# Optimization experiments

Measured on AMD Instinct MI355X. Metric: run time of the kernel, lower is better.

The kernel has to match this reference:

```python
import jax, jax.numpy as jnp
import numpy as np

B, NQ, NK, D, H, DFF = 4, 1024, 1024, 1024, 16, 4096
DH = D // H
SCALE = 1.0 / np.sqrt(D).astype(np.float32)  # torch code scales by sqrt(dim_V), not head_dim
LN_EPS = 1e-5


def setup_inputs() -> dict:
    key = jax.random.key(0)
    ks = jax.random.split(key, 20)
    s = lambda fan_in: 1.0 / np.sqrt(fan_in).astype(np.float32)
    inp = {
        "Q": jax.random.normal(ks[0], (B, NQ, D), jnp.float32),
        "K": jax.random.normal(ks[1], (B, NK, D), jnp.float32),
        # attention projections (torch Linear stored here as [in, out])
        "Wq": jax.random.uniform(ks[2], (D, D), jnp.float32, -s(D), s(D)),
        "bq": jnp.zeros((D,), jnp.float32),
        "Wk": jax.random.uniform(ks[3], (D, D), jnp.float32, -s(D), s(D)),
        "bk": jnp.zeros((D,), jnp.float32),
        "Wv": jax.random.uniform(ks[4], (D, D), jnp.float32, -s(D), s(D)),
        "bv": jnp.zeros((D,), jnp.float32),
        "Wo": jax.random.uniform(ks[5], (D, D), jnp.float32, -s(D), s(D)),
        "bo": jnp.zeros((D,), jnp.float32),
        # FFN
        "W1": jax.random.uniform(ks[6], (D, DFF), jnp.float32, -s(D), s(D)),
        "b1": jnp.zeros((DFF,), jnp.float32),
        "W2": jax.random.uniform(ks[7], (DFF, D), jnp.float32, -s(DFF), s(DFF)),
        "b2": jnp.zeros((D,), jnp.float32),
        # LayerNorms
        "g0": jnp.ones((D,), jnp.float32),
        "be0": jnp.zeros((D,), jnp.float32),
        "g1": jnp.ones((D,), jnp.float32),
        "be1": jnp.zeros((D,), jnp.float32),
    }
    return inp


def _layernorm(x, g, b):
    mu = x.mean(-1, keepdims=True)
    var = ((x - mu) ** 2).mean(-1, keepdims=True)
    return (x - mu) * jax.lax.rsqrt(var + LN_EPS) * g + b


def reference(Q, K, Wq, bq, Wk, bk, Wv, bv, Wo, bo, W1, b1, W2, b2, g0, be0, g1, be1):
    # multi-head attention (MHA path, mask=None)
    q = (Q @ Wq + bq).reshape(B, NQ, H, DH)
    k = (K @ Wk + bk).reshape(B, NK, H, DH)
    v = (K @ Wv + bv).reshape(B, NK, H, DH)
    E = jnp.einsum("bqhd,bkhd->bhqk", q, k) * SCALE  # [B,H,NQ,NK]
    A = jax.nn.softmax(E, axis=-1)
    O = jnp.einsum("bhqk,bkhd->bqhd", A, v).reshape(B, NQ, D)
    O = O @ Wo + bo
    # residual + LN0
    X = _layernorm(Q + O, g0, be0)
    # FFN + residual + LN1
    Y = jnp.maximum(X @ W1 + b1, 0.0) @ W2 + b2
    return _layernorm(X + Y, g1, be1)
```

## Files before the change

kernel.cpp:

```cpp
#include <hip/hip_runtime.h>
#include <math.h>

#define B_   4
#define NQ_  1024
#define NK_  1024
#define D_   1024
#define H_   16
#define DH_  64
#define DFF_ 4096
#define SCALE_ (1.0f/32.0f)
#define LN_EPS_ 1e-5f

typedef __attribute__((ext_vector_type(8))) short bf16x8_t;
typedef __attribute__((ext_vector_type(4))) float f32x4_t;

__device__ __forceinline__ ushort f2bf_rne(float x) {
    unsigned u = __float_as_uint(x);
    unsigned r = (u + 0x7FFFu + ((u >> 16) & 1u)) >> 16;
    return (ushort)r;
}
__device__ __forceinline__ float bf2f(ushort h) {
    return __uint_as_float(((unsigned)h) << 16);
}

__device__ __forceinline__ void gl_lds16(const ushort* g, ushort* l) {
    __builtin_amdgcn_global_load_lds(
        (const __attribute__((address_space(1))) unsigned int*)g,
        (__attribute__((address_space(3))) unsigned int*)l, 16, 0, 0);
}

__global__ __launch_bounds__(256) void split_rows(const float* __restrict__ src,
        ushort* __restrict__ hi, ushort* __restrict__ lo, int n4)
{
    int i = blockIdx.x * 256 + threadIdx.x;
    if (i >= n4) return;
    float4 v = ((const float4*)src)[i];
    ushort4 h, l;
    h.x = f2bf_rne(v.x); l.x = f2bf_rne(v.x - bf2f(h.x));
    h.y = f2bf_rne(v.y); l.y = f2bf_rne(v.y - bf2f(h.y));
    h.z = f2bf_rne(v.z); l.z = f2bf_rne(v.z - bf2f(h.z));
    h.w = f2bf_rne(v.w); l.w = f2bf_rne(v.w - bf2f(h.w));
    ((ushort4*)hi)[i] = h;
    ((ushort4*)lo)[i] = l;
}

__global__ __launch_bounds__(256) void split_tr(const float* __restrict__ Wsrc,
        ushort* __restrict__ th, ushort* __restrict__ tl, int K, int N)
{
    __shared__ float tile[32][33];
    const int nb = blockIdx.x * 32, kb = blockIdx.y * 32;
    const int t = threadIdx.x;
    {
        int r = t >> 3, c4 = (t & 7) * 4;
        float4 v = *(const float4*)&Wsrc[(size_t)(kb + r) * N + nb + c4];
        tile[r][c4 + 0] = v.x; tile[r][c4 + 1] = v.y;
        tile[r][c4 + 2] = v.z; tile[r][c4 + 3] = v.w;
    }
    __syncthreads();
    {
        int n = t >> 3, k4 = (t & 7) * 4;
        float a0 = tile[k4 + 0][n], a1 = tile[k4 + 1][n];
        float a2 = tile[k4 + 2][n], a3 = tile[k4 + 3][n];
        ushort4 h, l;
        h.x = f2bf_rne(a0); l.x = f2bf_rne(a0 - bf2f(h.x));
        h.y = f2bf_rne(a1); l.y = f2bf_rne(a1 - bf2f(h.y));
        h.z = f2bf_rne(a2); l.z = f2bf_rne(a2 - bf2f(h.z));
        h.w = f2bf_rne(a3); l.w = f2bf_rne(a3 - bf2f(h.w));
        size_t o = (size_t)(nb + n) * K + kb + k4;
        *(ushort4*)&th[o] = h;
        *(ushort4*)&tl[o] = l;
    }
}

__device__ __forceinline__ void swz_block(int& brow, int& bcol, int tile) {
    const int nx  = gridDim.x;
    const int lin = blockIdx.y * nx + blockIdx.x;
    const int cpx = (nx * gridDim.y) >> 3;
    const int swz = (lin & 7) * cpx + (lin >> 3);
    brow = (swz / nx) * tile;
    bcol = (swz % nx) * tile;
}

template<bool RELU, int OMODE>
__device__ __forceinline__ void gemm_body(
        const ushort* __restrict__ Ah, const ushort* __restrict__ Al,
        const ushort* __restrict__ Bh, const ushort* __restrict__ Bl,
        const float* __restrict__ bias,
        float* __restrict__ C, ushort* __restrict__ Ch, ushort* __restrict__ Cl,
        int M, int N, int Kd, int Klen, int brow, int bcol)
{
    __shared__ __align__(16) ushort S[2][4][128 * 32];

    const int t    = threadIdx.x;
    const int lane = t & 63;
    const int w    = t >> 6;
    const int wr   = (w >> 1) * 64;
    const int wc   = (w & 1) * 64;
    const int fr   = lane & 15;
    const int g    = lane >> 4;
    const int sS   = ((g ^ ((fr >> 1) & 3)) << 3);
    const int cl   = lane & 15;
    const int rq   = (lane >> 4) * 4;

    float bpre[4];
    #pragma unroll
    for (int j = 0; j < 4; ++j)
        bpre[j] = bias ? bias[bcol + wc + j * 16 + cl] : 0.f;

    f32x4_t acc[4][4];
    #pragma unroll
    for (int i = 0; i < 4; ++i)
        #pragma unroll
        for (int j = 0; j < 4; ++j)
            acc[i][j] = (f32x4_t){0.f, 0.f, 0.f, 0.f};

    const int lrow  = lane >> 2;
    const int lslot = ((lane & 3) ^ ((lane >> 3) & 3)) << 3;
    const int c0    = w * 2;

    auto issue2 = [&](const ushort* gpp, int rb, int pl, int buf, int k0) {
        #pragma unroll
        for (int ii = 0; ii < 2; ++ii) {
            int c = c0 + ii;
            gl_lds16(gpp + (size_t)(rb + c * 16 + lrow) * Kd + k0 + lslot,
                     &S[buf][pl][c * 512]);
        }
    };

    bf16x8_t ahf[4], bhf[4], blf[4], alf[4];

    issue2(Ah, brow, 0, 0, 0);
    issue2(Bh, bcol, 2, 0, 0);
    issue2(Bl, bcol, 3, 0, 0);
    issue2(Al, brow, 1, 0, 0);
    asm volatile("s_waitcnt vmcnt(4)" ::: "memory");
    __builtin_amdgcn_s_barrier();

    const int NT = Klen >> 5;
    for (int tt = 0; tt < NT; ++tt) {
        const int cur = tt & 1, nxt = cur ^ 1;
        const int kn  = (tt + 1) << 5;
        const bool more = (tt + 1 < NT);

        #pragma unroll
        for (int i = 0; i < 4; ++i)
            ahf[i] = *(const bf16x8_t*)&S[cur][0][(wr + i * 16 + fr) * 32 + sS];
        #pragma unroll
        for (int j = 0; j < 4; ++j)
            bhf[j] = *(const bf16x8_t*)&S[cur][2][(wc + j * 16 + fr) * 32 + sS];
        if (more) {
            issue2(Ah, brow, 0, nxt, kn);
            issue2(Bh, bcol, 2, nxt, kn);
            asm volatile("s_waitcnt vmcnt(6)" ::: "memory");
        } else {
            asm volatile("s_waitcnt vmcnt(2)" ::: "memory");
        }
        __builtin_amdgcn_s_barrier();
        asm volatile("s_waitcnt lgkmcnt(0)" ::: "memory");
        __builtin_amdgcn_sched_barrier(0);
        __builtin_amdgcn_s_setprio(1);
        #pragma unroll
        for (int i = 0; i < 4; ++i)
            #pragma unroll
            for (int j = 0; j < 4; ++j)
                acc[i][j] = __builtin_amdgcn_mfma_f32_16x16x32_bf16(ahf[i], bhf[j], acc[i][j], 0, 0, 0);
        __builtin_amdgcn_s_setprio(0);
        __builtin_amdgcn_s_barrier();

        #pragma unroll
        for (int j = 0; j < 4; ++j)
            blf[j] = *(const bf16x8_t*)&S[cur][3][(wc + j * 16 + fr) * 32 + sS];
        if (more) {
            issue2(Bl, bcol, 3, nxt, kn);
            asm volatile("s_waitcnt vmcnt(6)" ::: "memory");
        } else {
            asm volatile("s_waitcnt vmcnt(0)" ::: "memory");
        }
        __builtin_amdgcn_s_barrier();
        asm volatile("s_waitcnt lgkmcnt(0)" ::: "memory");
        __builtin_amdgcn_sched_barrier(0);
        __builtin_amdgcn_s_setprio(1);
        #pragma unroll
        for (int i = 0; i < 4; ++i)
            #pragma unroll
            for (int j = 0; j < 4; ++j)
                acc[i][j] = __builtin_amdgcn_mfma_f32_16x16x32_bf16(ahf[i], blf[j], acc[i][j], 0, 0, 0);
        __builtin_amdgcn_s_setprio(0);
        __builtin_amdgcn_s_barrier();

        #pragma unroll
        for (int i = 0; i < 4; ++i)
            alf[i] = *(const bf16x8_t*)&S[cur][1][(wr + i * 16 + fr) * 32 + sS];
        if (more) {
            issue2(Al, brow, 1, nxt, kn);
            asm volatile("s_waitcnt vmcnt(4)" ::: "memory");
        }
        __builtin_amdgcn_s_barrier();
        asm volatile("s_waitcnt lgkmcnt(0)" ::: "memory");
        __builtin_amdgcn_sched_barrier(0);
        __builtin_amdgcn_s_setprio(1);
        #pragma unroll
        for (int i = 0; i < 4; ++i)
            #pragma unroll
            for (int j = 0; j < 4; ++j)
                acc[i][j] = __builtin_amdgcn_mfma_f32_16x16x32_bf16(alf[i], bhf[j], acc[i][j], 0, 0, 0);
        __builtin_amdgcn_s_setprio(0);
        __builtin_amdgcn_s_barrier();
    }

    if (OMODE == 0) {
        #pragma unroll
        for (int j = 0; j < 4; ++j) {
            int col = bcol + wc + j * 16 + cl;
            #pragma unroll
            for (int i = 0; i < 4; ++i)
                #pragma unroll
                for (int r = 0; r < 4; ++r) {
                    int row = brow + wr + i * 16 + rq + r;
                    float v = acc[i][j][r] + bpre[j];
                    if (RELU) v = fmaxf(v, 0.f);
                    C[(size_t)row * N + col] = v;
                }
        }
    } else {
        float* E = (float*)&S[0][0][0] + w * 4096;
        #pragma unroll
        for (int j = 0; j < 4; ++j) {
            #pragma unroll
            for (int i = 0; i < 4; ++i)
                #pragma unroll
                for (int r = 0; r < 4; ++r) {
                    float v = acc[i][j][r] + bpre[j];
                    if (RELU) v = fmaxf(v, 0.f);
                    E[(i * 16 + rq + r) * 64 + j * 16 + cl] = v;
                }
        }
        __syncthreads();
        const int rr8 = lane >> 3;
        const int c8  = (lane & 7) * 8;
        #pragma unroll
        for (int p = 0; p < 8; ++p) {
            int rl = p * 8 + rr8;
            float4 va = *(float4*)&E[rl * 64 + c8];
            float4 vb = *(float4*)&E[rl * 64 + c8 + 4];
            float v[8] = {va.x, va.y, va.z, va.w, vb.x, vb.y, vb.z, vb.w};
            bf16x8_t hv, lv;
            #pragma unroll
            for (int q = 0; q < 8; ++q) {
                ushort hh = f2bf_rne(v[q]);
                hv[q] = (short)hh;
                lv[q] = (short)f2bf_rne(v[q] - bf2f(hh));
            }
            size_t o = (size_t)(brow + wr + rl) * N + (bcol + wc + c8);
            *(bf16x8_t*)&Ch[o] = hv;
            if (OMODE == 1) *(bf16x8_t*)&Cl[o] = lv;
        }
    }
}

template<bool RELU, int OMODE>
__global__ __launch_bounds__(256) void gemm_mfma(
        const ushort* __restrict__ Ah, const ushort* __restrict__ Al,
        const ushort* __restrict__ Bh, const ushort* __restrict__ Bl,
        const float* __restrict__ bias,
        float* __restrict__ C, ushort* __restrict__ Ch, ushort* __restrict__ Cl,
        int M, int N, int Kd)
{
    int brow, bcol;
    swz_block(brow, bcol, 128);
    gemm_body<RELU, OMODE>(Ah, Al, Bh, Bl, bias, C, Ch, Cl, M, N, Kd, Kd, brow, bcol);
}

__global__ __launch_bounds__(256) void gemm_splitk2(
        const ushort* __restrict__ Ah, const ushort* __restrict__ Al,
        const ushort* __restrict__ Bh, const ushort* __restrict__ Bl,
        const float* __restrict__ bias,
        float* __restrict__ C0, float* __restrict__ C1,
        int M, int N, int Kd)
{
    int brow, bcol;
    swz_block(brow, bcol, 128);
    const int z = blockIdx.z;
    const int Kh2 = Kd >> 1;
    const int ko  = z * Kh2;
    gemm_body<false, 0>(Ah + ko, Al + ko, Bh + ko, Bl + ko,
                        z == 0 ? bias : nullptr,
                        z == 0 ? C0 : C1, nullptr, nullptr,
                        M, N, Kd, Kh2, brow, bcol);
}

struct QkvArgs {
    const ushort* Ah[3]; const ushort* Al[3];
    const ushort* Bh[3]; const ushort* Bl[3];
    const float*  bias[3];
    ushort*       Co[3];
};

__global__ __launch_bounds__(256) void gemm_qkv(QkvArgs qa, int M, int N, int Kd)
{
    int brow, bcol;
    swz_block(brow, bcol, 128);
    const int z = blockIdx.z;
    gemm_body<false, 2>(qa.Ah[z], qa.Al[z], qa.Bh[z], qa.Bl[z], qa.bias[z],
                        nullptr, qa.Co[z], nullptr, M, N, Kd, Kd, brow, bcol);
}

__global__ __launch_bounds__(512) void gemm_ffn1_256(
        const ushort* __restrict__ Ah, const ushort* __restrict__ Al,
        const ushort* __restrict__ Bh, const ushort* __restrict__ Bl,
        const float* __restrict__ bias,
        ushort* __restrict__ Ch, ushort* __restrict__ Cl,
        int M, int N, int Kd)
{
    __shared__ __align__(16) ushort S[2][4][256 * 32];

    const int t    = threadIdx.x;
    const int lane = t & 63;
    const int w    = t >> 6;
    const int wr   = (w >> 2) * 128;
    const int wc   = (w & 3) * 64;
    const int fr   = lane & 15;
    const int g    = lane >> 4;
    const int sS   = ((g ^ ((fr >> 1) & 3)) << 3);
    const int cl   = lane & 15;
    const int rq   = (lane >> 4) * 4;

    int brow, bcol;
    swz_block(brow, bcol, 256);

    float bpre[4];
    #pragma unroll
    for (int j = 0; j < 4; ++j) bpre[j] = bias[bcol + wc + j * 16 + cl];

    f32x4_t acc[8][4];
    #pragma unroll
    for (int i = 0; i < 8; ++i)
        #pragma unroll
        for (int j = 0; j < 4; ++j)
            acc[i][j] = (f32x4_t){0.f, 0.f, 0.f, 0.f};

    const int lrow  = lane >> 2;
    const int lslot = ((lane & 3) ^ ((lane >> 3) & 3)) << 3;
    const int c0    = w * 2;

    auto issue2 = [&](const ushort* gpp, int rb, int pl, int buf, int k0) {
        #pragma unroll
        for (int ii = 0; ii < 2; ++ii) {
            int c = c0 + ii;
            gl_lds16(gpp + (size_t)(rb + c * 16 + lrow) * Kd + k0 + lslot,
                     &S[buf][pl][c * 512]);
        }
    };

    bf16x8_t ahf[8], bhf[4], blf[4], alf[8];

    issue2(Ah, brow, 0, 0, 0);
    issue2(Bh, bcol, 2, 0, 0);
    issue2(Bl, bcol, 3, 0, 0);
    issue2(Al, brow, 1, 0, 0);
    asm volatile("s_waitcnt vmcnt(4)" ::: "memory");
    __builtin_amdgcn_s_barrier();

    const int NT = Kd >> 5;
    for (int tt = 0; tt < NT; ++tt) {
        const int cur = tt & 1, nxt = cur ^ 1;
        const int kn  = (tt + 1) << 5;
        const bool more = (tt + 1 < NT);

        #pragma unroll
        for (int i = 0; i < 8; ++i)
            ahf[i] = *(const bf16x8_t*)&S[cur][0][(wr + i * 16 + fr) * 32 + sS];
        #pragma unroll
        for (int j = 0; j < 4; ++j)
            bhf[j] = *(const bf16x8_t*)&S[cur][2][(wc + j * 16 + fr) * 32 + sS];
        if (more) {
            issue2(Ah, brow, 0, nxt, kn);
            issue2(Bh, bcol, 2, nxt, kn);
            asm volatile("s_waitcnt vmcnt(6)" ::: "memory");
        } else {
            asm volatile("s_waitcnt vmcnt(2)" ::: "memory");
        }
        __builtin_amdgcn_s_barrier();
        asm volatile("s_waitcnt lgkmcnt(0)" ::: "memory");
        __builtin_amdgcn_sched_barrier(0);
        __builtin_amdgcn_s_setprio(1);
        #pragma unroll
        for (int i = 0; i < 8; ++i)
            #pragma unroll
            for (int j = 0; j < 4; ++j)
                acc[i][j] = __builtin_amdgcn_mfma_f32_16x16x32_bf16(ahf[i], bhf[j], acc[i][j], 0, 0, 0);
        __builtin_amdgcn_s_setprio(0);
        __builtin_amdgcn_s_barrier();

        #pragma unroll
        for (int j = 0; j < 4; ++j)
            blf[j] = *(const bf16x8_t*)&S[cur][3][(wc + j * 16 + fr) * 32 + sS];
        if (more) {
            issue2(Bl, bcol, 3, nxt, kn);
            asm volatile("s_waitcnt vmcnt(6)" ::: "memory");
        } else {
            asm volatile("s_waitcnt vmcnt(0)" ::: "memory");
        }
        __builtin_amdgcn_s_barrier();
        asm volatile("s_waitcnt lgkmcnt(0)" ::: "memory");
        __builtin_amdgcn_sched_barrier(0);
        __builtin_amdgcn_s_setprio(1);
        #pragma unroll
        for (int i = 0; i < 8; ++i)
            #pragma unroll
            for (int j = 0; j < 4; ++j)
                acc[i][j] = __builtin_amdgcn_mfma_f32_16x16x32_bf16(ahf[i], blf[j], acc[i][j], 0, 0, 0);
        __builtin_amdgcn_s_setprio(0);
        __builtin_amdgcn_s_barrier();

        #pragma unroll
        for (int i = 0; i < 8; ++i)
            alf[i] = *(const bf16x8_t*)&S[cur][1][(wr + i * 16 + fr) * 32 + sS];
        if (more) {
            issue2(Al, brow, 1, nxt, kn);
            asm volatile("s_waitcnt vmcnt(4)" ::: "memory");
        }
        __builtin_amdgcn_s_barrier();
        asm volatile("s_waitcnt lgkmcnt(0)" ::: "memory");
        __builtin_amdgcn_sched_barrier(0);
        __builtin_amdgcn_s_setprio(1);
        #pragma unroll
        for (int i = 0; i < 8; ++i)
            #pragma unroll
            for (int j = 0; j < 4; ++j)
                acc[i][j] = __builtin_amdgcn_mfma_f32_16x16x32_bf16(alf[i], bhf[j], acc[i][j], 0, 0, 0);
        __builtin_amdgcn_s_setprio(0);
        __builtin_amdgcn_s_barrier();
    }

    __syncthreads();
    float* E = (float*)&S[0][0][0] + w * 4096;
    const int rr8 = lane >> 3;
    const int c8  = (lane & 7) * 8;
    #pragma unroll
    for (int pass = 0; pass < 2; ++pass) {
        #pragma unroll
        for (int i = 0; i < 4; ++i) {
            #pragma unroll
            for (int j = 0; j < 4; ++j)
                #pragma unroll
                for (int r = 0; r < 4; ++r) {
                    float v = fmaxf(acc[pass * 4 + i][j][r] + bpre[j], 0.f);
                    E[(i * 16 + rq + r) * 64 + j * 16 + cl] = v;
                }
        }
        #pragma unroll
        for (int p = 0; p < 8; ++p) {
            int rl = p * 8 + rr8;
            float4 va = *(float4*)&E[rl * 64 + c8];
            float4 vb = *(float4*)&E[rl * 64 + c8 + 4];
            float v[8] = {va.x, va.y, va.z, va.w, vb.x, vb.y, vb.z, vb.w};
            bf16x8_t hv, lv;
            #pragma unroll
            for (int q = 0; q < 8; ++q) {
                ushort hh = f2bf_rne(v[q]);
                hv[q] = (short)hh;
                lv[q] = (short)f2bf_rne(v[q] - bf2f(hh));
            }
            size_t o = (size_t)(brow + wr + pass * 64 + rl) * N + (bcol + wc + c8);
            *(bf16x8_t*)&Ch[o] = hv;
            *(bf16x8_t*)&Cl[o] = lv;
        }
    }
}

__global__ __launch_bounds__(256) void flash_attn_mfma(
        const ushort* __restrict__ qh, const ushort* __restrict__ kh,
        const ushort* __restrict__ vh,
        ushort* __restrict__ Oh, ushort* __restrict__ Ol)
{
    __shared__ __align__(16) ushort SMEM[8192];
    ushort* sk  = SMEM;
    ushort* svt = SMEM + 2304;
    ushort* pw0 = SMEM + 4864;

    const int bid  = blockIdx.x;
    const int slot = bid >> 3;
    const int bh   = (bid & 7) * 8 + (slot >> 4);
    const int qt   = slot & 15;
    const int b    = bh >> 4;
    const int h    = bh & 15;
    const int qb   = qt * 64;

    const int t = threadIdx.x, lane = t & 63, w = t >> 6;
    const int l15 = lane & 15, g = lane >> 4;

    bf16x8_t qf[2];
    {
        size_t qrow = ((size_t)(b * NQ_) + qb + w * 16 + l15) * D_ + h * DH_;
        qf[0] = *(const bf16x8_t*)&qh[qrow + 0  + 8 * g];
        qf[1] = *(const bf16x8_t*)&qh[qrow + 32 + 8 * g];
    }

    f32x4_t acc[4];
    #pragma unroll
    for (int dt = 0; dt < 4; ++dt) acc[dt] = (f32x4_t){0.f, 0.f, 0.f, 0.f};
    float m = -INFINITY, l = 0.0f;

    const int kkv = t >> 3,  kds = (t & 7) * 8;
    const int vkv = t & 31,  vds = (t >> 5) * 8;
    const size_t kvbase = (size_t)(b * NK_) * D_ + h * DH_;

    bf16x8_t kreg = *(const bf16x8_t*)&kh[kvbase + (size_t)kkv * D_ + kds];
    bf16x8_t vreg = *(const bf16x8_t*)&vh[kvbase + (size_t)vkv * D_ + vds];

    ushort* pw = pw0 + w * 640;

    for (int kt = 0; kt < NK_; kt += 32) {
        __syncthreads();
        *(bf16x8_t*)&sk[kkv * 72 + kds] = kreg;
        #pragma unroll
        for (int j = 0; j < 8; ++j)
            svt[(vds + j) * 40 + vkv] = (ushort)vreg[j];
        __syncthreads();
        if (kt + 32 < NK_) {
            kreg = *(const bf16x8_t*)&kh[kvbase + (size_t)(kt + 32 + kkv) * D_ + kds];
            vreg = *(const bf16x8_t*)&vh[kvbase + (size_t)(kt + 32 + vkv) * D_ + vds];
        }

        f32x4_t s0 = (f32x4_t){0.f,0.f,0.f,0.f};
        f32x4_t s1 = (f32x4_t){0.f,0.f,0.f,0.f};
        #pragma unroll
        for (int c = 0; c < 2; ++c) {
            bf16x8_t k0 = *(const bf16x8_t*)&sk[(l15     ) * 72 + 32 * c + 8 * g];
            bf16x8_t k1 = *(const bf16x8_t*)&sk[(l15 + 16) * 72 + 32 * c + 8 * g];
            s0 = __builtin_amdgcn_mfma_f32_16x16x32_bf16(k0, qf[c], s0, 0, 0, 0);
            s1 = __builtin_amdgcn_mfma_f32_16x16x32_bf16(k1, qf[c], s1, 0, 0, 0);
        }

        float e0[4], e1[4];
        #pragma unroll
        for (int r = 0; r < 4; ++r) { e0[r] = s0[r] * SCALE_; e1[r] = s1[r] * SCALE_; }
        float tmax = fmaxf(fmaxf(fmaxf(e0[0], e0[1]), fmaxf(e0[2], e0[3])),
                           fmaxf(fmaxf(e1[0], e1[1]), fmaxf(e1[2], e1[3])));
        tmax = fmaxf(tmax, __shfl_xor(tmax, 16, 64));
        tmax = fmaxf(tmax, __shfl_xor(tmax, 32, 64));
        float mn   = fmaxf(m, tmax);
        float corr = __expf(m - mn);
        float p0[4], p1[4];
        float ps = 0.f;
        #pragma unroll
        for (int r = 0; r < 4; ++r) {
            p0[r] = __expf(e0[r] - mn);
            p1[r] = __expf(e1[r] - mn);
            ps += p0[r] + p1[r];
        }
        ps += __shfl_xor(ps, 16, 64);
        ps += __shfl_xor(ps, 32, 64);
        l = l * corr + ps;
        m = mn;
        #pragma unroll
        for (int dt = 0; dt < 4; ++dt)
            #pragma unroll
            for (int r = 0; r < 4; ++r)
                acc[dt][r] *= corr;

        ushort4 pk0, pk1;
        pk0.x = f2bf_rne(p0[0]); pk0.y = f2bf_rne(p0[1]);
        pk0.z = f2bf_rne(p0[2]); pk0.w = f2bf_rne(p0[3]);
        pk1.x = f2bf_rne(p1[0]); pk1.y = f2bf_rne(p1[1]);
        pk1.z = f2bf_rne(p1[2]); pk1.w = f2bf_rne(p1[3]);
        *(ushort4*)&pw[l15 * 40 + 4 * g]      = pk0;
        *(ushort4*)&pw[l15 * 40 + 16 + 4 * g] = pk1;
        bf16x8_t pa = *(const bf16x8_t*)&pw[l15 * 40 + 8 * g];

        #pragma unroll
        for (int dt = 0; dt < 4; ++dt) {
            bf16x8_t vf = *(const bf16x8_t*)&svt[(16 * dt + l15) * 40 + 8 * g];
            acc[dt] = __builtin_amdgcn_mfma_f32_16x16x32_bf16(vf, pa, acc[dt], 0, 0, 0);
        }
    }

    __syncthreads();
    float invl = 1.0f / l;
    float* Ew = (float*)SMEM + w * 1024;
    #pragma unroll
    for (int dt = 0; dt < 4; ++dt)
        #pragma unroll
        for (int r = 0; r < 4; ++r)
            Ew[(16 * dt + 4 * g + r) * 16 + l15] = acc[dt][r] * invl;
    const int ql = lane >> 2;
    const int dc = (lane & 3) * 16;
    float ov[16];
    #pragma unroll
    for (int j = 0; j < 16; ++j) ov[j] = Ew[(dc + j) * 16 + ql];
    bf16x8_t hv0, hv1, lv0, lv1;
    #pragma unroll
    for (int j = 0; j < 8; ++j) {
        ushort ha = f2bf_rne(ov[j]);
        ushort hb = f2bf_rne(ov[8 + j]);
        hv0[j] = (short)ha; lv0[j] = (short)f2bf_rne(ov[j] - bf2f(ha));
        hv1[j] = (short)hb; lv1[j] = (short)f2bf_rne(ov[8 + j] - bf2f(hb));
    }
    size_t orow = ((size_t)(b * NQ_) + qb + w * 16 + ql) * D_ + h * DH_ + dc;
    *(bf16x8_t*)&Oh[orow]     = hv0;
    *(bf16x8_t*)&Oh[orow + 8] = hv1;
    *(bf16x8_t*)&Ol[orow]     = lv0;
    *(bf16x8_t*)&Ol[orow + 8] = lv1;
}

template<bool SPLIT>
__global__ __launch_bounds__(256) void add_ln3(const float* __restrict__ a0,
        const float* __restrict__ a1, const float* __restrict__ r,
        const float* __restrict__ g, const float* __restrict__ be,
        float* __restrict__ out, ushort* __restrict__ oh, ushort* __restrict__ ol)
{
    const int row = blockIdx.x;
    const int t = threadIdx.x;
    float vals[4];
    float s1 = 0.0f, s2 = 0.0f;
    #pragma unroll
    for (int i = 0; i < 4; ++i) {
        int col = t + i * 256;
        size_t o = (size_t)row * D_ + col;
        float vv = a0[o] + a1[o] + r[o];
        vals[i] = vv;
        s1 += vv;
        s2 += vv * vv;
    }
    #pragma unroll
    for (int off = 32; off > 0; off >>= 1) {
        s1 += __shfl_down(s1, off, 64);
        s2 += __shfl_down(s2, off, 64);
    }
    __shared__ float p1[4], p2[4];
    const int wave = t >> 6;
    if ((t & 63) == 0) { p1[wave] = s1; p2[wave] = s2; }
    __syncthreads();
    s1 = p1[0] + p1[1] + p1[2] + p1[3];
    s2 = p2[0] + p2[1] + p2[2] + p2[3];
    const float mean = s1 * (1.0f / D_);
    const float var  = s2 * (1.0f / D_) - mean * mean;
    const float rstd = rsqrtf(var + LN_EPS_);
    #pragma unroll
    for (int i = 0; i < 4; ++i) {
        int col = t + i * 256;
        float v = (vals[i] - mean) * rstd * g[col] + be[col];
        out[(size_t)row * D_ + col] = v;
        if (SPLIT) {
            ushort h = f2bf_rne(v);
            oh[(size_t)row * D_ + col] = h;
            ol[(size_t)row * D_ + col] = f2bf_rne(v - bf2f(h));
        }
    }
}

extern "C" void kernel_launch(void* const* d_in, const int* in_sizes, int n_in,
                              void* d_out, int out_size, void* d_ws, size_t ws_size,
                              hipStream_t stream)
{
    const float* Q   = (const float*)d_in[0];
    const float* K   = (const float*)d_in[1];
    const float* Wq  = (const float*)d_in[2];
    const float* bq  = (const float*)d_in[3];
    const float* Wk  = (const float*)d_in[4];
    const float* bk  = (const float*)d_in[5];
    const float* Wv  = (const float*)d_in[6];
    const float* bv  = (const float*)d_in[7];
    const float* Wo  = (const float*)d_in[8];
    const float* bo  = (const float*)d_in[9];
    const float* W1  = (const float*)d_in[10];
    const float* b1  = (const float*)d_in[11];
    const float* W2  = (const float*)d_in[12];
    const float* b2  = (const float*)d_in[13];
    const float* g0  = (const float*)d_in[14];
    const float* be0 = (const float*)d_in[15];
    const float* g1  = (const float*)d_in[16];
    const float* be1 = (const float*)d_in[17];

    unsigned char* Wb = (unsigned char*)d_ws;
    const size_t MBy = 1ull << 20;

    ushort* Qh   = (ushort*)(Wb +  0 * MBy);
    ushort* Ql   = (ushort*)(Wb +  8 * MBy);
    ushort* Kh   = (ushort*)(Wb + 16 * MBy);
    ushort* Kl   = (ushort*)(Wb + 24 * MBy);
    ushort* Wqh  = (ushort*)(Wb + 32 * MBy);
    ushort* Wql  = (ushort*)(Wb + 34 * MBy);
    ushort* Wkh  = (ushort*)(Wb + 36 * MBy);
    ushort* Wkl  = (ushort*)(Wb + 38 * MBy);
    ushort* Wvh  = (ushort*)(Wb + 40 * MBy);
    ushort* Wvl  = (ushort*)(Wb + 42 * MBy);
    ushort* Woh  = (ushort*)(Wb + 44 * MBy);
    ushort* Wol  = (ushort*)(Wb + 46 * MBy);
    ushort* qhp  = (ushort*)(Wb + 48 * MBy);
    ushort* khp  = (ushort*)(Wb + 56 * MBy);
    ushort* vhp  = (ushort*)(Wb + 64 * MBy);
    ushort* aOh  = (ushort*)(Wb + 72 * MBy);
    ushort* aOl  = (ushort*)(Wb + 80 * MBy);

    float*  oprj0 = (float*)(Wb + 16 * MBy);
    float*  oprj1 = (float*)(Wb + 56 * MBy);
    float*  Xf    = (float*)(Wb +  0 * MBy);
    ushort* Xh    = (ushort*)(Wb + 32 * MBy);
    ushort* Xl    = (ushort*)(Wb + 40 * MBy);
    ushort* W1h   = (ushort*)(Wb + 16 * MBy);
    ushort* W1l   = (ushort*)(Wb + 24 * MBy);
    ushort* Hih   = (ushort*)(Wb + 80 * MBy);
    ushort* Hil   = (ushort*)(Wb + 48 * MBy);
    ushort* W2h   = (ushort*)(Wb + 16 * MBy);
    ushort* W2l   = (ushort*)(Wb + 24 * MBy);
    float*  Y0    = (float*)(Wb + 32 * MBy);
    float*  Y1    = (float*)d_out;

    const int M = B_ * NQ_;
    const int n4act = M * D_ / 4;
    dim3 blk(256);
    dim3 gQKV(D_ / 128, M / 128, 3);
    dim3 gSK(D_ / 128, M / 128, 2);

    split_rows<<<n4act / 256, blk, 0, stream>>>(Q, Qh, Ql, n4act);
    split_rows<<<n4act / 256, blk, 0, stream>>>(K, Kh, Kl, n4act);
    split_tr<<<dim3(D_/32, D_/32), blk, 0, stream>>>(Wq, Wqh, Wql, D_, D_);
    split_tr<<<dim3(D_/32, D_/32), blk, 0, stream>>>(Wk, Wkh, Wkl, D_, D_);
    split_tr<<<dim3(D_/32, D_/32), blk, 0, stream>>>(Wv, Wvh, Wvl, D_, D_);
    split_tr<<<dim3(D_/32, D_/32), blk, 0, stream>>>(Wo, Woh, Wol, D_, D_);

    QkvArgs qa;
    qa.Ah[0] = Qh;  qa.Al[0] = Ql;  qa.Bh[0] = Wqh; qa.Bl[0] = Wql; qa.bias[0] = bq; qa.Co[0] = qhp;
    qa.Ah[1] = Kh;  qa.Al[1] = Kl;  qa.Bh[1] = Wkh; qa.Bl[1] = Wkl; qa.bias[1] = bk; qa.Co[1] = khp;
    qa.Ah[2] = Kh;  qa.Al[2] = Kl;  qa.Bh[2] = Wvh; qa.Bl[2] = Wvl; qa.bias[2] = bv; qa.Co[2] = vhp;
    gemm_qkv<<<gQKV, blk, 0, stream>>>(qa, M, D_, D_);

    flash_attn_mfma<<<dim3(1024), blk, 0, stream>>>(qhp, khp, vhp, aOh, aOl);

    gemm_splitk2<<<gSK, blk, 0, stream>>>(aOh, aOl, Woh, Wol, bo, oprj0, oprj1, M, D_, D_);
    add_ln3<true><<<M, blk, 0, stream>>>(oprj0, oprj1, Q, g0, be0, Xf, Xh, Xl);

    split_tr<<<dim3(DFF_/32, D_/32), blk, 0, stream>>>(W1, W1h, W1l, D_, DFF_);
    gemm_ffn1_256<<<dim3(DFF_/256, M/256), dim3(512), 0, stream>>>(
        Xh, Xl, W1h, W1l, b1, Hih, Hil, M, DFF_, D_);
    split_tr<<<dim3(D_/32, DFF_/32), blk, 0, stream>>>(W2, W2h, W2l, DFF_, D_);

    gemm_splitk2<<<gSK, blk, 0, stream>>>(Hih, Hil, W2h, W2l, b2, Y0, Y1, M, D_, DFF_);
    add_ln3<false><<<M, blk, 0, stream>>>(Y0, Y1, Xf, g1, be1, (float*)d_out, nullptr, nullptr);
}
```

Baseline: 396.9 us.

## Use 256x128 split-K GEMM tiles and batch split/transpose launches

Adds a 512-thread split-K GEMM that computes 256x128 output tiles for the Wo projection and the second FFN GEMM. It replaces the 128x128 split-K kernel and uses a staged hi/lo LDS pipeline with explicit waitcnt and barriers. It also merges the two activation split launches and the four weight split-transposes into single batched launches. The larger tile raises operand reuse and the merges cut launch overhead, but grid size per GEMM halves to 256 blocks, which may leave CUs underused.

```diff
diff --git a/kernel.cpp b/kernel.cpp
--- a/kernel.cpp
+++ b/kernel.cpp
@@ -29,22 +29,24 @@
         (__attribute__((address_space(3))) unsigned int*)l, 16, 0, 0);
 }
 
-__global__ __launch_bounds__(256) void split_rows(const float* __restrict__ src,
-        ushort* __restrict__ hi, ushort* __restrict__ lo, int n4)
+struct Rows2 { const float* src[2]; ushort* hi[2]; ushort* lo[2]; };
+
+__global__ __launch_bounds__(256) void split_rows2(Rows2 a, int n4)
 {
     int i = blockIdx.x * 256 + threadIdx.x;
     if (i >= n4) return;
-    float4 v = ((const float4*)src)[i];
+    const int z = blockIdx.z;
+    float4 v = ((const float4*)a.src[z])[i];
     ushort4 h, l;
     h.x = f2bf_rne(v.x); l.x = f2bf_rne(v.x - bf2f(h.x));
     h.y = f2bf_rne(v.y); l.y = f2bf_rne(v.y - bf2f(h.y));
     h.z = f2bf_rne(v.z); l.z = f2bf_rne(v.z - bf2f(h.z));
     h.w = f2bf_rne(v.w); l.w = f2bf_rne(v.w - bf2f(h.w));
-    ((ushort4*)hi)[i] = h;
-    ((ushort4*)lo)[i] = l;
-}
-
-__global__ __launch_bounds__(256) void split_tr(const float* __restrict__ Wsrc,
+    ((ushort4*)a.hi[z])[i] = h;
+    ((ushort4*)a.lo[z])[i] = l;
+}
+
+__device__ __forceinline__ void split_tr_body(const float* __restrict__ Wsrc,
         ushort* __restrict__ th, ushort* __restrict__ tl, int K, int N)
 {
     __shared__ float tile[32][33];
@@ -72,6 +74,20 @@
     }
 }
 
+__global__ __launch_bounds__(256) void split_tr(const float* __restrict__ Wsrc,
+        ushort* __restrict__ th, ushort* __restrict__ tl, int K, int N)
+{
+    split_tr_body(Wsrc, th, tl, K, N);
+}
+
+struct Tr4 { const float* w[4]; ushort* th[4]; ushort* tl[4]; };
+
+__global__ __launch_bounds__(256) void split_tr4(Tr4 a)
+{
+    const int z = blockIdx.z;
+    split_tr_body(a.w[z], a.th[z], a.tl[z], D_, D_);
+}
+
 __device__ __forceinline__ void swz_block(int& brow, int& bcol, int tile) {
     const int nx  = gridDim.x;
     const int lin = blockIdx.y * nx + blockIdx.x;
@@ -258,37 +274,6 @@
     }
 }
 
-template<bool RELU, int OMODE>
-__global__ __launch_bounds__(256) void gemm_mfma(
-        const ushort* __restrict__ Ah, const ushort* __restrict__ Al,
-        const ushort* __restrict__ Bh, const ushort* __restrict__ Bl,
-        const float* __restrict__ bias,
-        float* __restrict__ C, ushort* __restrict__ Ch, ushort* __restrict__ Cl,
-        int M, int N, int Kd)
-{
-    int brow, bcol;
-    swz_block(brow, bcol, 128);
-    gemm_body<RELU, OMODE>(Ah, Al, Bh, Bl, bias, C, Ch, Cl, M, N, Kd, Kd, brow, bcol);
-}
-
-__global__ __launch_bounds__(256) void gemm_splitk2(
-        const ushort* __restrict__ Ah, const ushort* __restrict__ Al,
-        const ushort* __restrict__ Bh, const ushort* __restrict__ Bl,
-        const float* __restrict__ bias,
-        float* __restrict__ C0, float* __restrict__ C1,
-        int M, int N, int Kd)
-{
-    int brow, bcol;
-    swz_block(brow, bcol, 128);
-    const int z = blockIdx.z;
-    const int Kh2 = Kd >> 1;
-    const int ko  = z * Kh2;
-    gemm_body<false, 0>(Ah + ko, Al + ko, Bh + ko, Bl + ko,
-                        z == 0 ? bias : nullptr,
-                        z == 0 ? C0 : C1, nullptr, nullptr,
-                        M, N, Kd, Kh2, brow, bcol);
-}
-
 struct QkvArgs {
     const ushort* Ah[3]; const ushort* Al[3];
     const ushort* Bh[3]; const ushort* Bl[3];
@@ -303,6 +288,170 @@
     const int z = blockIdx.z;
     gemm_body<false, 2>(qa.Ah[z], qa.Al[z], qa.Bh[z], qa.Bl[z], qa.bias[z],
                         nullptr, qa.Co[z], nullptr, M, N, Kd, Kd, brow, bcol);
+}
+
+__global__ __launch_bounds__(512) void gemm_sk2_256(
+        const ushort* __restrict__ Ah_, const ushort* __restrict__ Al_,
+        const ushort* __restrict__ Bh_, const ushort* __restrict__ Bl_,
+        const float* __restrict__ bias_,
+        float* __restrict__ C0, float* __restrict__ C1,
+        int M, int N, int Kd)
+{
+    __shared__ __align__(16) ushort SA[2][2][256 * 32];
+    __shared__ __align__(16) ushort SB[2][2][128 * 32];
+
+    const int z   = blockIdx.z;
+    const int Kh2 = Kd >> 1;
+    const int ko  = z * Kh2;
+    const ushort* Ah = Ah_ + ko;
+    const ushort* Al = Al_ + ko;
+    const ushort* Bh = Bh_ + ko;
+    const ushort* Bl = Bl_ + ko;
+    const float*  bias = (z == 0) ? bias_ : nullptr;
+    float* C = (z == 0) ? C0 : C1;
+
+    const int t    = threadIdx.x;
+    const int lane = t & 63;
+    const int w    = t >> 6;
+    const int wr   = (w >> 1) * 64;
+    const int wc   = (w & 1) * 64;
+    const int fr   = lane & 15;
+    const int g    = lane >> 4;
+    const int sS   = ((g ^ ((fr >> 1) & 3)) << 3);
+    const int cl   = lane & 15;
+    const int rq   = (lane >> 4) * 4;
+
+    int brow, bcol;
+    {
+        const int nx  = gridDim.x;
+        const int lin = blockIdx.y * nx + blockIdx.x;
+        const int cpx = (nx * gridDim.y) >> 3;
+        const int swz = (lin & 7) * cpx + (lin >> 3);
+        brow = (swz / nx) * 256;
+        bcol = (swz % nx) * 128;
+    }
+
+    float bpre[4];
+    #pragma unroll
+    for (int j = 0; j < 4; ++j)
+        bpre[j] = bias ? bias[bcol + wc + j * 16 + cl] : 0.f;
+
+    f32x4_t acc[4][4];
+    #pragma unroll
+    for (int i = 0; i < 4; ++i)
+        #pragma unroll
+        for (int j = 0; j < 4; ++j)
+            acc[i][j] = (f32x4_t){0.f, 0.f, 0.f, 0.f};
+
+    const int lrow  = lane >> 2;
+    const int lslot = ((lane & 3) ^ ((lane >> 3) & 3)) << 3;
+    const int cA0   = w * 2;
+
+    auto issueA = [&](const ushort* gpp, int pl, int buf, int k0) {
+        #pragma unroll
+        for (int ii = 0; ii < 2; ++ii) {
+            int c = cA0 + ii;
+            gl_lds16(gpp + (size_t)(brow + c * 16 + lrow) * Kd + k0 + lslot,
+                     &SA[buf][pl][c * 512]);
+        }
+    };
+    auto issueB = [&](const ushort* gpp, int pl, int buf, int k0) {
+        gl_lds16(gpp + (size_t)(bcol + w * 16 + lrow) * Kd + k0 + lslot,
+                 &SB[buf][pl][w * 512]);
+    };
+
+    bf16x8_t ahf[4], bhf[4], blf[4], alf[4];
+
+    issueA(Ah, 0, 0, 0);
+    issueB(Bh, 0, 0, 0);
+    issueB(Bl, 1, 0, 0);
+    issueA(Al, 1, 0, 0);
+    asm volatile("s_waitcnt vmcnt(3)" ::: "memory");
+    __builtin_amdgcn_s_barrier();
+
+    const int NT = Kh2 >> 5;
+    for (int tt = 0; tt < NT; ++tt) {
+        const int cur = tt & 1, nxt = cur ^ 1;
+        const int kn  = (tt + 1) << 5;
+        const bool more = (tt + 1 < NT);
+
+        #pragma unroll
+        for (int i = 0; i < 4; ++i)
+            ahf[i] = *(const bf16x8_t*)&SA[cur][0][(wr + i * 16 + fr) * 32 + sS];
+        #pragma unroll
+        for (int j = 0; j < 4; ++j)
+            bhf[j] = *(const bf16x8_t*)&SB[cur][0][(wc + j * 16 + fr) * 32 + sS];
+        if (more) {
+            issueA(Ah, 0, nxt, kn);
+            issueB(Bh, 0, nxt, kn);
+            asm volatile("s_waitcnt vmcnt(5)" ::: "memory");
+        } else {
+            asm volatile("s_waitcnt vmcnt(2)" ::: "memory");
+        }
+        __builtin_amdgcn_s_barrier();
+        asm volatile("s_waitcnt lgkmcnt(0)" ::: "memory");
+        __builtin_amdgcn_sched_barrier(0);
+        __builtin_amdgcn_s_setprio(1);
+        #pragma unroll
+        for (int i = 0; i < 4; ++i)
+            #pragma unroll
+            for (int j = 0; j < 4; ++j)
+                acc[i][j] = __builtin_amdgcn_mfma_f32_16x16x32_bf16(ahf[i], bhf[j], acc[i][j], 0, 0, 0);
+        __builtin_amdgcn_s_setprio(0);
+        __builtin_amdgcn_s_barrier();
+
+        #pragma unroll
+        for (int j = 0; j < 4; ++j)
+            blf[j] = *(const bf16x8_t*)&SB[cur][1][(wc + j * 16 + fr) * 32 + sS];
+        if (more) {
+            issueB(Bl, 1, nxt, kn);
+            asm volatile("s_waitcnt vmcnt(4)" ::: "memory");
+        } else {
+            asm volatile("s_waitcnt vmcnt(0)" ::: "memory");
+        }
+        __builtin_amdgcn_s_barrier();
+        asm volatile("s_waitcnt lgkmcnt(0)" ::: "memory");
+        __builtin_amdgcn_sched_barrier(0);
+        __builtin_amdgcn_s_setprio(1);
+        #pragma unroll
+        for (int i = 0; i < 4; ++i)
+            #pragma unroll
+            for (int j = 0; j < 4; ++j)
+                acc[i][j] = __builtin_amdgcn_mfma_f32_16x16x32_bf16(ahf[i], blf[j], acc[i][j], 0, 0, 0);
+        __builtin_amdgcn_s_setprio(0);
+        __builtin_amdgcn_s_barrier();
+
+        #pragma unroll
+        for (int i = 0; i < 4; ++i)
+            alf[i] = *(const bf16x8_t*)&SA[cur][1][(wr + i * 16 + fr) * 32 + sS];
+        if (more) {
+            issueA(Al, 1, nxt, kn);
+            asm volatile("s_waitcnt vmcnt(3)" ::: "memory");
+        }
+        __builtin_amdgcn_s_barrier();
+        asm volatile("s_waitcnt lgkmcnt(0)" ::: "memory");
+        __builtin_amdgcn_sched_barrier(0);
+        __builtin_amdgcn_s_setprio(1);
+        #pragma unroll
+        for (int i = 0; i < 4; ++i)
+            #pragma unroll
+            for (int j = 0; j < 4; ++j)
+                acc[i][j] = __builtin_amdgcn_mfma_f32_16x16x32_bf16(alf[i], bhf[j], acc[i][j], 0, 0, 0);
+        __builtin_amdgcn_s_setprio(0);
+        __builtin_amdgcn_s_barrier();
+    }
+
+    #pragma unroll
+    for (int j = 0; j < 4; ++j) {
+        int col = bcol + wc + j * 16 + cl;
+        #pragma unroll
+        for (int i = 0; i < 4; ++i)
+            #pragma unroll
+            for (int r = 0; r < 4; ++r) {
+                int row = brow + wr + i * 16 + rq + r;
+                C[(size_t)row * N + col] = acc[i][j][r] + bpre[j];
+            }
+    }
 }
 
 __global__ __launch_bounds__(512) void gemm_ffn1_256(
@@ -712,14 +861,19 @@
     const int n4act = M * D_ / 4;
     dim3 blk(256);
     dim3 gQKV(D_ / 128, M / 128, 3);
-    dim3 gSK(D_ / 128, M / 128, 2);
-
-    split_rows<<<n4act / 256, blk, 0, stream>>>(Q, Qh, Ql, n4act);
-    split_rows<<<n4act / 256, blk, 0, stream>>>(K, Kh, Kl, n4act);
-    split_tr<<<dim3(D_/32, D_/32), blk, 0, stream>>>(Wq, Wqh, Wql, D_, D_);
-    split_tr<<<dim3(D_/32, D_/32), blk, 0, stream>>>(Wk, Wkh, Wkl, D_, D_);
-    split_tr<<<dim3(D_/32, D_/32), blk, 0, stream>>>(Wv, Wvh, Wvl, D_, D_);
-    split_tr<<<dim3(D_/32, D_/32), blk, 0, stream>>>(Wo, Woh, Wol, D_, D_);
+    dim3 gSK256(D_ / 128, M / 256, 2);
+
+    Rows2 r2;
+    r2.src[0] = Q; r2.hi[0] = Qh; r2.lo[0] = Ql;
+    r2.src[1] = K; r2.hi[1] = Kh; r2.lo[1] = Kl;
+    split_rows2<<<dim3(n4act / 256, 1, 2), blk, 0, stream>>>(r2, n4act);
+
+    Tr4 t4;
+    t4.w[0] = Wq; t4.th[0] = Wqh; t4.tl[0] = Wql;
+    t4.w[1] = Wk; t4.th[1] = Wkh; t4.tl[1] = Wkl;
+    t4.w[2] = Wv; t4.th[2] = Wvh; t4.tl[2] = Wvl;
+    t4.w[3] = Wo; t4.th[3] = Woh; t4.tl[3] = Wol;
+    split_tr4<<<dim3(D_/32, D_/32, 4), blk, 0, stream>>>(t4);
 
     QkvArgs qa;
     qa.Ah[0] = Qh;  qa.Al[0] = Ql;  qa.Bh[0] = Wqh; qa.Bl[0] = Wql; qa.bias[0] = bq; qa.Co[0] = qhp;
@@ -729,7 +883,8 @@
 
     flash_attn_mfma<<<dim3(1024), blk, 0, stream>>>(qhp, khp, vhp, aOh, aOl);
 
-    gemm_splitk2<<<gSK, blk, 0, stream>>>(aOh, aOl, Woh, Wol, bo, oprj0, oprj1, M, D_, D_);
+    gemm_sk2_256<<<gSK256, dim3(512), 0, stream>>>(aOh, aOl, Woh, Wol, bo,
+                                                   oprj0, oprj1, M, D_, D_);
     add_ln3<true><<<M, blk, 0, stream>>>(oprj0, oprj1, Q, g0, be0, Xf, Xh, Xl);
 
     split_tr<<<dim3(DFF_/32, D_/32), blk, 0, stream>>>(W1, W1h, W1l, D_, DFF_);
@@ -737,6 +892,7 @@
         Xh, Xl, W1h, W1l, b1, Hih, Hil, M, DFF_, D_);
     split_tr<<<dim3(D_/32, DFF_/32), blk, 0, stream>>>(W2, W2h, W2l, DFF_, D_);
 
-    gemm_splitk2<<<gSK, blk, 0, stream>>>(Hih, Hil, W2h, W2l, b2, Y0, Y1, M, D_, DFF_);
+    gemm_sk2_256<<<gSK256, dim3(512), 0, stream>>>(Hih, Hil, W2h, W2l, b2,
+                                                   Y0, Y1, M, D_, DFF_);
     add_ln3<false><<<M, blk, 0, stream>>>(Y0, Y1, Xf, g1, be1, (float*)d_out, nullptr, nullptr);
 }
```

Result: no change. 402.8 us (+1.5%).

## Widen flash-attention KV tile to 64 and batch split kernels into fewer launches

Applied to the files above, without the earlier changes.

The flash attention kernel now processes 64 keys per iteration instead of 32. That halves the number of loop iterations and barrier pairs and gives each wave more MFMA work per softmax rescale, at the cost of more LDS and registers. Separately, the two row-split launches and the four weight-transpose-split launches are merged into single launches indexed by blockIdx.z, which removes launch overhead and small-grid tail effects. The unused gemm_mfma template is deleted.

```diff
diff --git a/kernel.cpp b/kernel.cpp
--- a/kernel.cpp
+++ b/kernel.cpp
@@ -29,22 +29,24 @@
         (__attribute__((address_space(3))) unsigned int*)l, 16, 0, 0);
 }
 
-__global__ __launch_bounds__(256) void split_rows(const float* __restrict__ src,
-        ushort* __restrict__ hi, ushort* __restrict__ lo, int n4)
+struct Rows2 { const float* src[2]; ushort* hi[2]; ushort* lo[2]; };
+
+__global__ __launch_bounds__(256) void split_rows2(Rows2 a, int n4)
 {
     int i = blockIdx.x * 256 + threadIdx.x;
     if (i >= n4) return;
-    float4 v = ((const float4*)src)[i];
+    const int z = blockIdx.z;
+    float4 v = ((const float4*)a.src[z])[i];
     ushort4 h, l;
     h.x = f2bf_rne(v.x); l.x = f2bf_rne(v.x - bf2f(h.x));
     h.y = f2bf_rne(v.y); l.y = f2bf_rne(v.y - bf2f(h.y));
     h.z = f2bf_rne(v.z); l.z = f2bf_rne(v.z - bf2f(h.z));
     h.w = f2bf_rne(v.w); l.w = f2bf_rne(v.w - bf2f(h.w));
-    ((ushort4*)hi)[i] = h;
-    ((ushort4*)lo)[i] = l;
-}
-
-__global__ __launch_bounds__(256) void split_tr(const float* __restrict__ Wsrc,
+    ((ushort4*)a.hi[z])[i] = h;
+    ((ushort4*)a.lo[z])[i] = l;
+}
+
+__device__ __forceinline__ void split_tr_body(const float* __restrict__ Wsrc,
         ushort* __restrict__ th, ushort* __restrict__ tl, int K, int N)
 {
     __shared__ float tile[32][33];
@@ -72,6 +74,20 @@
     }
 }
 
+__global__ __launch_bounds__(256) void split_tr(const float* __restrict__ Wsrc,
+        ushort* __restrict__ th, ushort* __restrict__ tl, int K, int N)
+{
+    split_tr_body(Wsrc, th, tl, K, N);
+}
+
+struct Tr4 { const float* w[4]; ushort* th[4]; ushort* tl[4]; };
+
+__global__ __launch_bounds__(256) void split_tr4(Tr4 a)
+{
+    const int z = blockIdx.z;
+    split_tr_body(a.w[z], a.th[z], a.tl[z], D_, D_);
+}
+
 __device__ __forceinline__ void swz_block(int& brow, int& bcol, int tile) {
     const int nx  = gridDim.x;
     const int lin = blockIdx.y * nx + blockIdx.x;
@@ -258,19 +274,6 @@
     }
 }
 
-template<bool RELU, int OMODE>
-__global__ __launch_bounds__(256) void gemm_mfma(
-        const ushort* __restrict__ Ah, const ushort* __restrict__ Al,
-        const ushort* __restrict__ Bh, const ushort* __restrict__ Bl,
-        const float* __restrict__ bias,
-        float* __restrict__ C, ushort* __restrict__ Ch, ushort* __restrict__ Cl,
-        int M, int N, int Kd)
-{
-    int brow, bcol;
-    swz_block(brow, bcol, 128);
-    gemm_body<RELU, OMODE>(Ah, Al, Bh, Bl, bias, C, Ch, Cl, M, N, Kd, Kd, brow, bcol);
-}
-
 __global__ __launch_bounds__(256) void gemm_splitk2(
         const ushort* __restrict__ Ah, const ushort* __restrict__ Al,
         const ushort* __restrict__ Bh, const ushort* __restrict__ Bl,
@@ -474,10 +477,10 @@
         const ushort* __restrict__ vh,
         ushort* __restrict__ Oh, ushort* __restrict__ Ol)
 {
-    __shared__ __align__(16) ushort SMEM[8192];
+    __shared__ __align__(16) ushort SMEM[13824];
     ushort* sk  = SMEM;
-    ushort* svt = SMEM + 2304;
-    ushort* pw0 = SMEM + 4864;
+    ushort* svt = SMEM + 4608;
+    ushort* pw0 = SMEM + 9216;
 
     const int bid  = blockIdx.x;
     const int slot = bid >> 3;
@@ -502,54 +505,64 @@
     for (int dt = 0; dt < 4; ++dt) acc[dt] = (f32x4_t){0.f, 0.f, 0.f, 0.f};
     float m = -INFINITY, l = 0.0f;
 
-    const int kkv = t >> 3,  kds = (t & 7) * 8;
-    const int vkv = t & 31,  vds = (t >> 5) * 8;
+    const int kkv = t >> 2;
+    const int kds = (t & 3) * 16;
+    const int vkv = t & 63;
+    const int vds = (t >> 6) * 16;
     const size_t kvbase = (size_t)(b * NK_) * D_ + h * DH_;
 
-    bf16x8_t kreg = *(const bf16x8_t*)&kh[kvbase + (size_t)kkv * D_ + kds];
-    bf16x8_t vreg = *(const bf16x8_t*)&vh[kvbase + (size_t)vkv * D_ + vds];
-
-    ushort* pw = pw0 + w * 640;
-
-    for (int kt = 0; kt < NK_; kt += 32) {
+    bf16x8_t kr0 = *(const bf16x8_t*)&kh[kvbase + (size_t)kkv * D_ + kds];
+    bf16x8_t kr1 = *(const bf16x8_t*)&kh[kvbase + (size_t)kkv * D_ + kds + 8];
+    bf16x8_t vr0 = *(const bf16x8_t*)&vh[kvbase + (size_t)vkv * D_ + vds];
+    bf16x8_t vr1 = *(const bf16x8_t*)&vh[kvbase + (size_t)vkv * D_ + vds + 8];
+
+    ushort* pw = pw0 + w * 1152;
+
+    for (int kt = 0; kt < NK_; kt += 64) {
         __syncthreads();
-        *(bf16x8_t*)&sk[kkv * 72 + kds] = kreg;
-        #pragma unroll
-        for (int j = 0; j < 8; ++j)
-            svt[(vds + j) * 40 + vkv] = (ushort)vreg[j];
+        *(bf16x8_t*)&sk[kkv * 72 + kds]     = kr0;
+        *(bf16x8_t*)&sk[kkv * 72 + kds + 8] = kr1;
+        #pragma unroll
+        for (int j = 0; j < 8; ++j) {
+            svt[(vds + j)     * 72 + vkv] = (ushort)vr0[j];
+            svt[(vds + 8 + j) * 72 + vkv] = (ushort)vr1[j];
+        }
         __syncthreads();
-        if (kt + 32 < NK_) {
-            kreg = *(const bf16x8_t*)&kh[kvbase + (size_t)(kt + 32 + kkv) * D_ + kds];
-            vreg = *(const bf16x8_t*)&vh[kvbase + (size_t)(kt + 32 + vkv) * D_ + vds];
-        }
-
-        f32x4_t s0 = (f32x4_t){0.f,0.f,0.f,0.f};
-        f32x4_t s1 = (f32x4_t){0.f,0.f,0.f,0.f};
-        #pragma unroll
-        for (int c = 0; c < 2; ++c) {
-            bf16x8_t k0 = *(const bf16x8_t*)&sk[(l15     ) * 72 + 32 * c + 8 * g];
-            bf16x8_t k1 = *(const bf16x8_t*)&sk[(l15 + 16) * 72 + 32 * c + 8 * g];
-            s0 = __builtin_amdgcn_mfma_f32_16x16x32_bf16(k0, qf[c], s0, 0, 0, 0);
-            s1 = __builtin_amdgcn_mfma_f32_16x16x32_bf16(k1, qf[c], s1, 0, 0, 0);
-        }
-
-        float e0[4], e1[4];
-        #pragma unroll
-        for (int r = 0; r < 4; ++r) { e0[r] = s0[r] * SCALE_; e1[r] = s1[r] * SCALE_; }
-        float tmax = fmaxf(fmaxf(fmaxf(e0[0], e0[1]), fmaxf(e0[2], e0[3])),
-                           fmaxf(fmaxf(e1[0], e1[1]), fmaxf(e1[2], e1[3])));
+        if (kt + 64 < NK_) {
+            kr0 = *(const bf16x8_t*)&kh[kvbase + (size_t)(kt + 64 + kkv) * D_ + kds];
+            kr1 = *(const bf16x8_t*)&kh[kvbase + (size_t)(kt + 64 + kkv) * D_ + kds + 8];
+            vr0 = *(const bf16x8_t*)&vh[kvbase + (size_t)(kt + 64 + vkv) * D_ + vds];
+            vr1 = *(const bf16x8_t*)&vh[kvbase + (size_t)(kt + 64 + vkv) * D_ + vds + 8];
+        }
+
+        f32x4_t s[4];
+        #pragma unroll
+        for (int tq = 0; tq < 4; ++tq) s[tq] = (f32x4_t){0.f,0.f,0.f,0.f};
+        #pragma unroll
+        for (int c = 0; c < 2; ++c)
+            #pragma unroll
+            for (int tq = 0; tq < 4; ++tq) {
+                bf16x8_t kf = *(const bf16x8_t*)&sk[(l15 + 16 * tq) * 72 + 32 * c + 8 * g];
+                s[tq] = __builtin_amdgcn_mfma_f32_16x16x32_bf16(kf, qf[c], s[tq], 0, 0, 0);
+            }
+
+        float e[16];
+        #pragma unroll
+        for (int tq = 0; tq < 4; ++tq)
+            #pragma unroll
+            for (int r = 0; r < 4; ++r)
+                e[4 * tq + r] = s[tq][r] * SCALE_;
+        float tmax = e[0];
+        #pragma unroll
+        for (int i = 1; i < 16; ++i) tmax = fmaxf(tmax, e[i]);
         tmax = fmaxf(tmax, __shfl_xor(tmax, 16, 64));
         tmax = fmaxf(tmax, __shfl_xor(tmax, 32, 64));
         float mn   = fmaxf(m, tmax);
         float corr = __expf(m - mn);
-        float p0[4], p1[4];
+        float p[16];
         float ps = 0.f;
         #pragma unroll
-        for (int r = 0; r < 4; ++r) {
-            p0[r] = __expf(e0[r] - mn);
-            p1[r] = __expf(e1[r] - mn);
-            ps += p0[r] + p1[r];
-        }
+        for (int i = 0; i < 16; ++i) { p[i] = __expf(e[i] - mn); ps += p[i]; }
         ps += __shfl_xor(ps, 16, 64);
         ps += __shfl_xor(ps, 32, 64);
         l = l * corr + ps;
@@ -560,19 +573,22 @@
             for (int r = 0; r < 4; ++r)
                 acc[dt][r] *= corr;
 
-        ushort4 pk0, pk1;
-        pk0.x = f2bf_rne(p0[0]); pk0.y = f2bf_rne(p0[1]);
-        pk0.z = f2bf_rne(p0[2]); pk0.w = f2bf_rne(p0[3]);
-        pk1.x = f2bf_rne(p1[0]); pk1.y = f2bf_rne(p1[1]);
-        pk1.z = f2bf_rne(p1[2]); pk1.w = f2bf_rne(p1[3]);
-        *(ushort4*)&pw[l15 * 40 + 4 * g]      = pk0;
-        *(ushort4*)&pw[l15 * 40 + 16 + 4 * g] = pk1;
-        bf16x8_t pa = *(const bf16x8_t*)&pw[l15 * 40 + 8 * g];
+        #pragma unroll
+        for (int tq = 0; tq < 4; ++tq) {
+            ushort4 pk;
+            pk.x = f2bf_rne(p[4 * tq + 0]); pk.y = f2bf_rne(p[4 * tq + 1]);
+            pk.z = f2bf_rne(p[4 * tq + 2]); pk.w = f2bf_rne(p[4 * tq + 3]);
+            *(ushort4*)&pw[l15 * 72 + 16 * tq + 4 * g] = pk;
+        }
+        bf16x8_t pa0 = *(const bf16x8_t*)&pw[l15 * 72 + 8 * g];
+        bf16x8_t pa1 = *(const bf16x8_t*)&pw[l15 * 72 + 32 + 8 * g];
 
         #pragma unroll
         for (int dt = 0; dt < 4; ++dt) {
-            bf16x8_t vf = *(const bf16x8_t*)&svt[(16 * dt + l15) * 40 + 8 * g];
-            acc[dt] = __builtin_amdgcn_mfma_f32_16x16x32_bf16(vf, pa, acc[dt], 0, 0, 0);
+            bf16x8_t vf0 = *(const bf16x8_t*)&svt[(16 * dt + l15) * 72 + 8 * g];
+            bf16x8_t vf1 = *(const bf16x8_t*)&svt[(16 * dt + l15) * 72 + 32 + 8 * g];
+            acc[dt] = __builtin_amdgcn_mfma_f32_16x16x32_bf16(vf0, pa0, acc[dt], 0, 0, 0);
+            acc[dt] = __builtin_amdgcn_mfma_f32_16x16x32_bf16(vf1, pa1, acc[dt], 0, 0, 0);
         }
     }
 
@@ -714,12 +730,17 @@
     dim3 gQKV(D_ / 128, M / 128, 3);
     dim3 gSK(D_ / 128, M / 128, 2);
 
-    split_rows<<<n4act / 256, blk, 0, stream>>>(Q, Qh, Ql, n4act);
-    split_rows<<<n4act / 256, blk, 0, stream>>>(K, Kh, Kl, n4act);
-    split_tr<<<dim3(D_/32, D_/32), blk, 0, stream>>>(Wq, Wqh, Wql, D_, D_);
-    split_tr<<<dim3(D_/32, D_/32), blk, 0, stream>>>(Wk, Wkh, Wkl, D_, D_);
-    split_tr<<<dim3(D_/32, D_/32), blk, 0, stream>>>(Wv, Wvh, Wvl, D_, D_);
-    split_tr<<<dim3(D_/32, D_/32), blk, 0, stream>>>(Wo, Woh, Wol, D_, D_);
+    Rows2 r2;
+    r2.src[0] = Q; r2.hi[0] = Qh; r2.lo[0] = Ql;
+    r2.src[1] = K; r2.hi[1] = Kh; r2.lo[1] = Kl;
+    split_rows2<<<dim3(n4act / 256, 1, 2), blk, 0, stream>>>(r2, n4act);
+
+    Tr4 t4;
+    t4.w[0] = Wq; t4.th[0] = Wqh; t4.tl[0] = Wql;
+    t4.w[1] = Wk; t4.th[1] = Wkh; t4.tl[1] = Wkl;
+    t4.w[2] = Wv; t4.th[2] = Wvh; t4.tl[2] = Wvl;
+    t4.w[3] = Wo; t4.th[3] = Woh; t4.tl[3] = Wol;
+    split_tr4<<<dim3(D_/32, D_/32, 4), blk, 0, stream>>>(t4);
 
     QkvArgs qa;
     qa.Ah[0] = Qh;  qa.Al[0] = Ql;  qa.Bh[0] = Wqh; qa.Bl[0] = Wql; qa.bias[0] = bq; qa.Co[0] = qhp;
```

Result: faster. 385.7 us (-2.8%).
